# Optimization experiments

Hardware: AMD Instinct MI355X
Metric: run time of the kernel (lower is better)

## Reference

```python
import jax, jax.numpy as jnp
import numpy as np

EPS = 1e-5  # BatchNorm2d eps; BN in eval mode with running_mean=0, running_var=1

def conv_bn_relu(x, W, g, b):
    # x: [B, Cin, N, K]; W: [Cout, Cin] (1x1 conv). BN eval: (y-0)/sqrt(1+eps)*g + b, then ReLU.
    y = jnp.einsum('oc,bcnk->bonk', W, x)
    scale = (g / jnp.sqrt(1.0 + EPS))[None, :, None, None]
    return jax.nn.relu(y * scale + b[None, :, None, None])

def gather_neighbour(pc, idx):
    # pc: [B, N, d]; idx: [B, N, K] -> [B, N, K, d]
    B, N, K = idx.shape
    flat = idx.reshape(B, N * K, 1)
    return jnp.take_along_axis(pc, flat, axis=1).reshape(B, N, K, pc.shape[-1])

def setup_inputs() -> dict:
    B, N, K, D, H = 4, 40960, 16, 64, 32  # H = D // rfa_param
    key = jax.random.key(0)
    ks = jax.random.split(key, 16)
    inp = {
        'feature': jax.random.normal(ks[0], (B, D, N, 1), jnp.float32),
        'xyz': jax.random.normal(ks[1], (B, N, 3), jnp.float32),
        'neigh_idx': jax.random.randint(ks[2], (B, N, K), 0, N, jnp.int64),
        'W1': jax.random.normal(ks[3], (H, 10), jnp.float32) * 0.1,
        'W2': jax.random.normal(ks[4], (H, D), jnp.float32) * 0.1,
        'W3': jax.random.normal(ks[5], (H, 2 * H), jnp.float32) * 0.1,
        'W4': jax.random.normal(ks[6], (D, 2 * H), jnp.float32) * 0.1,
    }
    for i, h in zip(range(1, 5), (H, H, H, D)):
        inp[f'g{i}'] = jax.random.uniform(ks[6 + i], (h,), jnp.float32) + 0.5
        inp[f'b{i}'] = jax.random.normal(ks[10 + i], (h,), jnp.float32) * 0.1
    return inp

def reference(feature, xyz, W1, g1, b1, W2, g2, b2, W3, g3, b3, W4, g4, b4, neigh_idx):
    B, N, K = neigh_idx.shape
    # relative position encoding -> [B, N, K, 10]
    neighbor_xyz = gather_neighbour(xyz, neigh_idx)
    xyz_tile = jnp.broadcast_to(xyz[:, :, None, :], (B, N, K, 3))
    relative_xyz = xyz_tile - neighbor_xyz
    relative_dis = jnp.sqrt(jnp.sum(relative_xyz ** 2, axis=-1, keepdims=True))
    f_xyz = jnp.concatenate([relative_dis, relative_xyz, xyz_tile, neighbor_xyz], axis=-1)
    f_xyz = jnp.transpose(f_xyz, (0, 3, 1, 2))          # [B, 10, N, K]
    f_xyz = conv_bn_relu(f_xyz, W1, g1, b1)             # [B, H, N, K]
    f = conv_bn_relu(feature, W2, g2, b2)               # [B, H, N, 1]
    f_pts = jnp.transpose(f[..., 0], (0, 2, 1))         # [B, N, H]
    f_neighbours = gather_neighbour(f_pts, neigh_idx)   # [B, N, K, H]
    f_neighbours = jnp.transpose(f_neighbours, (0, 3, 1, 2))  # [B, H, N, K]
    f_concat = jnp.concatenate([f_neighbours, f_xyz], axis=1)  # [B, 2H, N, K]
    f_concat = conv_bn_relu(f_concat, W3, g3, b3)       # [B, H, N, K]
    f_concat = jnp.max(f_concat, axis=3, keepdims=True)  # max pooling over neighbors
    f = jnp.concatenate([f_concat, f], axis=1)          # [B, 2H, N, 1]
    return conv_bn_relu(f, W4, g4, b4)                  # [B, D, N, 1]
```

## Files before the change

kernel.cpp:

```cpp
#include <hip/hip_runtime.h>
#include <math.h>

typedef __bf16 bf16_t;
typedef bf16_t bf16x8 __attribute__((ext_vector_type(8)));
typedef bf16_t bf16x4 __attribute__((ext_vector_type(4)));
typedef float  f32x4  __attribute__((ext_vector_type(4)));

#define MFMA16(a, b, c) __builtin_amdgcn_mfma_f32_16x16x32_bf16(a, b, c, 0, 0, 0)

constexpr float BN_INV = 0.999995000037499687f;
constexpr int G2 = 2;

__global__ __launch_bounds__(256) void rfa_k1(
    const float* __restrict__ feature, const float* __restrict__ xyz,
    const float* __restrict__ W2,
    const float* __restrict__ g2, const float* __restrict__ b2,
    bf16_t* __restrict__ fbf, float4* __restrict__ xyz4,
    int N, int nwaves)
{
    int gtid = blockIdx.x * 256 + threadIdx.x;
    int w = gtid >> 6, lane = gtid & 63;
    if (w >= nwaves) return;
    int pt = lane & 15, quad = lane >> 4;
    int T0 = w * 64;
    int b  = T0 / N;
    int n0 = T0 - b * N;

    {
        size_t p = (size_t)T0 + lane;
        xyz4[p] = make_float4(xyz[p * 3], xyz[p * 3 + 1], xyz[p * 3 + 2], 0.f);
    }

    bf16x8 A[2][2];
    #pragma unroll
    for (int mt = 0; mt < 2; ++mt) {
        int h = mt * 16 + pt;
        float sc = g2[h] * BN_INV;
        #pragma unroll
        for (int ks = 0; ks < 2; ++ks) {
            const float* src = W2 + h * 64 + ks * 32 + quad * 8;
            bf16x8 v;
            #pragma unroll
            for (int j = 0; j < 8; ++j) v[j] = (bf16_t)(src[j] * sc);
            A[mt][ks] = v;
        }
    }
    float b2r[8];
    #pragma unroll
    for (int mt = 0; mt < 2; ++mt)
        #pragma unroll
        for (int r = 0; r < 4; ++r) b2r[mt * 4 + r] = b2[mt * 16 + quad * 4 + r];

    const float* fb = feature + (size_t)b * 64 * N;

    #pragma unroll
    for (int g = 0; g < 4; ++g) {
        int nn = n0 + g * 16 + pt;
        size_t T = (size_t)T0 + g * 16 + pt;
        bf16x8 Bf[2];
        #pragma unroll
        for (int ks = 0; ks < 2; ++ks) {
            bf16x8 v;
            #pragma unroll
            for (int j = 0; j < 8; ++j)
                v[j] = (bf16_t)fb[(size_t)(ks * 32 + quad * 8 + j) * N + nn];
            Bf[ks] = v;
        }
        f32x4 acc[2] = {f32x4{0,0,0,0}, f32x4{0,0,0,0}};
        #pragma unroll
        for (int mt = 0; mt < 2; ++mt) {
            acc[mt] = MFMA16(A[mt][0], Bf[0], acc[mt]);
            acc[mt] = MFMA16(A[mt][1], Bf[1], acc[mt]);
        }
        #pragma unroll
        for (int mt = 0; mt < 2; ++mt) {
            bf16x4 o;
            #pragma unroll
            for (int r = 0; r < 4; ++r)
                o[r] = (bf16_t)fmaxf(acc[mt][r] + b2r[mt * 4 + r], 0.f);
            *(bf16x4*)(fbf + T * 32 + mt * 16 + quad * 4) = o;
        }
    }
}

__global__ __launch_bounds__(256) void rfa_k2(
    const float4* __restrict__ xyz4, const int* __restrict__ nidx,
    const float* __restrict__ W1, const float* __restrict__ g1, const float* __restrict__ b1,
    const float* __restrict__ W3, const float* __restrict__ g3, const float* __restrict__ b3,
    const float* __restrict__ W4, const float* __restrict__ g4, const float* __restrict__ b4,
    const bf16_t* __restrict__ fbf, float* __restrict__ out,
    int N, int ngroups)
{
    __shared__ __align__(16) bf16_t sW4[8 * 64 * 8];
    __shared__ float sB[4][32 * 18];

    int tid = threadIdx.x;
    for (int s = tid; s < 512; s += 256) {
        int f = s >> 6, l = s & 63;
        int mt = f >> 1, ks = f & 1, nn = l & 15, q = l >> 4;
        int o = mt * 16 + nn;
        float sc = g4[o] * BN_INV;
        const float* src = W4 + o * 64 + ks * 32 + q * 8;
        bf16x8 v;
        #pragma unroll
        for (int j = 0; j < 8; ++j) v[j] = (bf16_t)(src[j] * sc);
        *(bf16x8*)(sW4 + s * 8) = v;
    }
    __syncthreads();

    int lane = tid & 63, wv = tid >> 6;
    int n = lane & 15, quad = lane >> 4;

    bf16x8 A3[2][2];
    #pragma unroll
    for (int mt = 0; mt < 2; ++mt) {
        int h = mt * 16 + n;
        float sc = g3[h] * BN_INV;
        #pragma unroll
        for (int ks = 0; ks < 2; ++ks) {
            const float* src = W3 + h * 64 + ks * 32 + quad * 8;
            bf16x8 v;
            #pragma unroll
            for (int j = 0; j < 8; ++j) v[j] = (bf16_t)(src[j] * sc);
            A3[mt][ks] = v;
        }
    }
    float a8[8], V0[8], V1[8], V2[8];
    #pragma unroll
    for (int j = 0; j < 8; ++j) {
        int c = quad * 8 + j;
        float s1 = g1[c] * BN_INV;
        const float* wp = W1 + c * 10;
        a8[j] = wp[0] * s1;
        V0[j] = (wp[7] - wp[1]) * s1;
        V1[j] = (wp[8] - wp[2]) * s1;
        V2[j] = (wp[9] - wp[3]) * s1;
    }
    float b3r[8];
    #pragma unroll
    for (int mt = 0; mt < 2; ++mt)
        #pragma unroll
        for (int r = 0; r < 4; ++r) b3r[mt * 4 + r] = b3[mt * 16 + quad * 4 + r];

    float* bounce = sB[wv];
    int wave_id = blockIdx.x * 4 + wv;

    for (int gi = 0; gi < G2; ++gi) {
        int grp = wave_id * G2 + gi;
        if (grp >= ngroups) break;
        int t0 = grp * 16;
        int b = t0 / N;
        int base = b * N;
        int nloc = t0 - base;

        float4 ps = xyz4[(size_t)t0 + n];
        float hoist[8];
        #pragma unroll
        for (int j = 0; j < 8; ++j) {
            int c = quad * 8 + j;
            float s1 = g1[c] * BN_INV;
            const float* wp = W1 + c * 10;
            hoist[j] = b1[c] + ((wp[1] + wp[4]) * ps.x + (wp[2] + wp[5]) * ps.y +
                                (wp[3] + wp[6]) * ps.z) * s1;
        }
        int4 myidx = *(const int4*)(nidx + (size_t)(t0 + n) * 16 + quad * 4);
        bf16x8 Bs = *(const bf16x8*)(fbf + (size_t)(t0 + n) * 32 + quad * 8);

        f32x4 mx0 = {-3.0e38f, -3.0e38f, -3.0e38f, -3.0e38f};
        f32x4 mx1 = {-3.0e38f, -3.0e38f, -3.0e38f, -3.0e38f};

        #pragma unroll
        for (int k = 0; k < 16; ++k) {
            const int comp = k & 3;
            int src = (comp == 0) ? myidx.x : (comp == 1) ? myidx.y
                     : (comp == 2) ? myidx.z : myidx.w;
            int j = __builtin_amdgcn_ds_bpermute(n * 4 + (k >> 2) * 64, src);

            float4 pn = xyz4[(size_t)base + j];
            float rx = ps.x - pn.x, ry = ps.y - pn.y, rz = ps.z - pn.z;
            float dist = sqrtf(rx * rx + ry * ry + rz * rz);

            bf16x8 Bx;
            #pragma unroll
            for (int c = 0; c < 8; ++c) {
                float v = hoist[c] + a8[c] * dist;
                v = fmaf(V0[c], pn.x, v);
                v = fmaf(V1[c], pn.y, v);
                v = fmaf(V2[c], pn.z, v);
                Bx[c] = (bf16_t)fmaxf(v, 0.f);
            }
            bf16x8 Bj = *(const bf16x8*)(fbf + (size_t)(base + j) * 32 + quad * 8);

            f32x4 ac0 = {0,0,0,0}, ac1 = {0,0,0,0};
            ac0 = MFMA16(A3[0][0], Bj, ac0);
            ac0 = MFMA16(A3[0][1], Bx, ac0);
            ac1 = MFMA16(A3[1][0], Bj, ac1);
            ac1 = MFMA16(A3[1][1], Bx, ac1);
            #pragma unroll
            for (int r = 0; r < 4; ++r) {
                mx0[r] = fmaxf(mx0[r], ac0[r]);
                mx1[r] = fmaxf(mx1[r], ac1[r]);
            }
        }

        #pragma unroll
        for (int r = 0; r < 4; ++r) {
            bounce[(quad * 4 + r) * 18 + n]      = fmaxf(mx0[r] + b3r[r], 0.f);
            bounce[(16 + quad * 4 + r) * 18 + n] = fmaxf(mx1[r] + b3r[4 + r], 0.f);
        }
        asm volatile("s_waitcnt lgkmcnt(0)" ::: "memory");
        bf16x8 Bm;
        #pragma unroll
        for (int jj = 0; jj < 8; ++jj)
            Bm[jj] = (bf16_t)bounce[(quad * 8 + jj) * 18 + n];

        #pragma unroll
        for (int mt = 0; mt < 4; ++mt) {
            bf16x8 A40 = *(const bf16x8*)(sW4 + ((size_t)(mt * 2 + 0) * 64 + lane) * 8);
            bf16x8 A41 = *(const bf16x8*)(sW4 + ((size_t)(mt * 2 + 1) * 64 + lane) * 8);
            f32x4 acc = {0,0,0,0};
            acc = MFMA16(A40, Bm, acc);
            acc = MFMA16(A41, Bs, acc);
            #pragma unroll
            for (int r = 0; r < 4; ++r) {
                int o = mt * 16 + quad * 4 + r;
                out[((size_t)b * 64 + o) * N + nloc + n] = fmaxf(acc[r] + b4[o], 0.f);
            }
        }
        asm volatile("s_waitcnt lgkmcnt(0)" ::: "memory");
    }
}

extern "C" void kernel_launch(void* const* d_in, const int* in_sizes, int n_in,
                              void* d_out, int out_size, void* d_ws, size_t ws_size,
                              hipStream_t stream) {
    const float* feature = (const float*)d_in[0];
    const float* xyz     = (const float*)d_in[1];
    const int*   nidx    = (const int*)  d_in[2];
    const float* W1      = (const float*)d_in[3];
    const float* W2      = (const float*)d_in[4];
    const float* W3      = (const float*)d_in[5];
    const float* W4      = (const float*)d_in[6];
    const float* g1 = (const float*)d_in[7];
    const float* b1 = (const float*)d_in[8];
    const float* g2 = (const float*)d_in[9];
    const float* b2 = (const float*)d_in[10];
    const float* g3 = (const float*)d_in[11];
    const float* b3 = (const float*)d_in[12];
    const float* g4 = (const float*)d_in[13];
    const float* b4 = (const float*)d_in[14];
    float* out = (float*)d_out;

    const int B = 4;
    const int N = in_sizes[1] / (B * 3);
    const int total = B * N;

    bf16_t* fbf  = (bf16_t*)d_ws;
    float4* xyz4 = (float4*)((char*)d_ws + (size_t)total * 32 * sizeof(bf16_t));

    const int nw1 = total / 64;
    const int blk1 = (nw1 + 3) / 4;
    const int ngroups = total / 16;
    const int nw2 = (ngroups + G2 - 1) / G2;
    const int blk2 = (nw2 + 3) / 4;

    rfa_k1<<<blk1, 256, 0, stream>>>(feature, xyz, W2, g2, b2, fbf, xyz4, N, nw1);
    rfa_k2<<<blk2, 256, 0, stream>>>(xyz4, nidx, W1, g1, b1, W3, g3, b3, W4, g4, b4,
                                     fbf, out, N, ngroups);
}
```

Before: 193.5 us.

## Interleave features and xyz into 128-byte records and prefetch neighbour gathers

Packs each point's bf16 feature vector (64 B) and padded xyz (16 B) into one 128-byte record, so a neighbour gather touches a single cache line instead of two separate arrays. Each lane now loads all 16 neighbour indices directly instead of exchanging them through ds_bpermute, and the gathers are double-buffered two steps ahead of the MFMA compute to hide memory latency. The cost is more registers for the index array and prefetch buffers, plus padding bytes in the workspace.

```diff
diff --git a/kernel.cpp b/kernel.cpp
--- a/kernel.cpp
+++ b/kernel.cpp
@@ -10,13 +10,13 @@
 
 constexpr float BN_INV = 0.999995000037499687f;
 constexpr int G2 = 2;
+constexpr int RECB = 128;
 
 __global__ __launch_bounds__(256) void rfa_k1(
     const float* __restrict__ feature, const float* __restrict__ xyz,
     const float* __restrict__ W2,
     const float* __restrict__ g2, const float* __restrict__ b2,
-    bf16_t* __restrict__ fbf, float4* __restrict__ xyz4,
-    int N, int nwaves)
+    char* __restrict__ rec, int N, int nwaves)
 {
     int gtid = blockIdx.x * 256 + threadIdx.x;
     int w = gtid >> 6, lane = gtid & 63;
@@ -28,7 +28,8 @@
 
     {
         size_t p = (size_t)T0 + lane;
-        xyz4[p] = make_float4(xyz[p * 3], xyz[p * 3 + 1], xyz[p * 3 + 2], 0.f);
+        float4 v = make_float4(xyz[p * 3], xyz[p * 3 + 1], xyz[p * 3 + 2], 0.f);
+        *(float4*)(rec + p * RECB + 64) = v;
     }
 
     bf16x8 A[2][2];
@@ -78,18 +79,17 @@
             #pragma unroll
             for (int r = 0; r < 4; ++r)
                 o[r] = (bf16_t)fmaxf(acc[mt][r] + b2r[mt * 4 + r], 0.f);
-            *(bf16x4*)(fbf + T * 32 + mt * 16 + quad * 4) = o;
+            *(bf16x4*)(rec + T * RECB + (mt * 16 + quad * 4) * 2) = o;
         }
     }
 }
 
 __global__ __launch_bounds__(256) void rfa_k2(
-    const float4* __restrict__ xyz4, const int* __restrict__ nidx,
+    const char* __restrict__ rec, const int* __restrict__ nidx,
     const float* __restrict__ W1, const float* __restrict__ g1, const float* __restrict__ b1,
     const float* __restrict__ W3, const float* __restrict__ g3, const float* __restrict__ b3,
     const float* __restrict__ W4, const float* __restrict__ g4, const float* __restrict__ b4,
-    const bf16_t* __restrict__ fbf, float* __restrict__ out,
-    int N, int ngroups)
+    float* __restrict__ out, int N, int ngroups)
 {
     __shared__ __align__(16) bf16_t sW4[8 * 64 * 8];
     __shared__ float sB[4][32 * 18];
@@ -136,11 +136,6 @@
         V1[j] = (wp[8] - wp[2]) * s1;
         V2[j] = (wp[9] - wp[3]) * s1;
     }
-    float b3r[8];
-    #pragma unroll
-    for (int mt = 0; mt < 2; ++mt)
-        #pragma unroll
-        for (int r = 0; r < 4; ++r) b3r[mt * 4 + r] = b3[mt * 16 + quad * 4 + r];
 
     float* bounce = sB[wv];
     int wave_id = blockIdx.x * 4 + wv;
@@ -153,7 +148,10 @@
         int base = b * N;
         int nloc = t0 - base;
 
-        float4 ps = xyz4[(size_t)t0 + n];
+        const char* recb  = rec + (size_t)base * RECB;
+        const char* selfr = rec + (size_t)(t0 + n) * RECB;
+
+        float4 ps = *(const float4*)(selfr + 64);
         float hoist[8];
         #pragma unroll
         for (int j = 0; j < 8; ++j) {
@@ -163,33 +161,46 @@
             hoist[j] = b1[c] + ((wp[1] + wp[4]) * ps.x + (wp[2] + wp[5]) * ps.y +
                                 (wp[3] + wp[6]) * ps.z) * s1;
         }
-        int4 myidx = *(const int4*)(nidx + (size_t)(t0 + n) * 16 + quad * 4);
-        bf16x8 Bs = *(const bf16x8*)(fbf + (size_t)(t0 + n) * 32 + quad * 8);
+
+        int j16[16];
+        #pragma unroll
+        for (int q4 = 0; q4 < 4; ++q4) {
+            int4 v = *(const int4*)(nidx + (size_t)(t0 + n) * 16 + q4 * 4);
+            j16[q4 * 4 + 0] = v.x; j16[q4 * 4 + 1] = v.y;
+            j16[q4 * 4 + 2] = v.z; j16[q4 * 4 + 3] = v.w;
+        }
+
+        bf16x8 fj[2]; float4 pn[2];
+        {
+            const char* rp0 = recb + (size_t)j16[0] * RECB;
+            const char* rp1 = recb + (size_t)j16[1] * RECB;
+            fj[0] = *(const bf16x8*)(rp0 + quad * 16);
+            pn[0] = *(const float4*)(rp0 + 64);
+            fj[1] = *(const bf16x8*)(rp1 + quad * 16);
+            pn[1] = *(const float4*)(rp1 + 64);
+        }
 
         f32x4 mx0 = {-3.0e38f, -3.0e38f, -3.0e38f, -3.0e38f};
         f32x4 mx1 = {-3.0e38f, -3.0e38f, -3.0e38f, -3.0e38f};
 
         #pragma unroll
         for (int k = 0; k < 16; ++k) {
-            const int comp = k & 3;
-            int src = (comp == 0) ? myidx.x : (comp == 1) ? myidx.y
-                     : (comp == 2) ? myidx.z : myidx.w;
-            int j = __builtin_amdgcn_ds_bpermute(n * 4 + (k >> 2) * 64, src);
-
-            float4 pn = xyz4[(size_t)base + j];
-            float rx = ps.x - pn.x, ry = ps.y - pn.y, rz = ps.z - pn.z;
+            int s = k & 1;
+            float4 p = pn[s];
+            bf16x8 Bj = fj[s];
+
+            float rx = ps.x - p.x, ry = ps.y - p.y, rz = ps.z - p.z;
             float dist = sqrtf(rx * rx + ry * ry + rz * rz);
 
             bf16x8 Bx;
             #pragma unroll
             for (int c = 0; c < 8; ++c) {
-                float v = hoist[c] + a8[c] * dist;
-                v = fmaf(V0[c], pn.x, v);
-                v = fmaf(V1[c], pn.y, v);
-                v = fmaf(V2[c], pn.z, v);
+                float v = fmaf(a8[c], dist, hoist[c]);
+                v = fmaf(V0[c], p.x, v);
+                v = fmaf(V1[c], p.y, v);
+                v = fmaf(V2[c], p.z, v);
                 Bx[c] = (bf16_t)fmaxf(v, 0.f);
             }
-            bf16x8 Bj = *(const bf16x8*)(fbf + (size_t)(base + j) * 32 + quad * 8);
 
             f32x4 ac0 = {0,0,0,0}, ac1 = {0,0,0,0};
             ac0 = MFMA16(A3[0][0], Bj, ac0);
@@ -201,7 +212,19 @@
                 mx0[r] = fmaxf(mx0[r], ac0[r]);
                 mx1[r] = fmaxf(mx1[r], ac1[r]);
             }
-        }
+
+            if (k + 2 < 16) {
+                const char* rp = recb + (size_t)j16[k + 2] * RECB;
+                fj[s] = *(const bf16x8*)(rp + quad * 16);
+                pn[s] = *(const float4*)(rp + 64);
+            }
+        }
+
+        float b3r[8];
+        #pragma unroll
+        for (int mt = 0; mt < 2; ++mt)
+            #pragma unroll
+            for (int r = 0; r < 4; ++r) b3r[mt * 4 + r] = b3[mt * 16 + quad * 4 + r];
 
         #pragma unroll
         for (int r = 0; r < 4; ++r) {
@@ -213,6 +236,8 @@
         #pragma unroll
         for (int jj = 0; jj < 8; ++jj)
             Bm[jj] = (bf16_t)bounce[(quad * 8 + jj) * 18 + n];
+
+        bf16x8 Bs = *(const bf16x8*)(selfr + quad * 16);
 
         #pragma unroll
         for (int mt = 0; mt < 4; ++mt) {
@@ -255,8 +280,7 @@
     const int N = in_sizes[1] / (B * 3);
     const int total = B * N;
 
-    bf16_t* fbf  = (bf16_t*)d_ws;
-    float4* xyz4 = (float4*)((char*)d_ws + (size_t)total * 32 * sizeof(bf16_t));
+    char* rec = (char*)d_ws;
 
     const int nw1 = total / 64;
     const int blk1 = (nw1 + 3) / 4;
@@ -264,7 +288,7 @@
     const int nw2 = (ngroups + G2 - 1) / G2;
     const int blk2 = (nw2 + 3) / 4;
 
-    rfa_k1<<<blk1, 256, 0, stream>>>(feature, xyz, W2, g2, b2, fbf, xyz4, N, nw1);
-    rfa_k2<<<blk2, 256, 0, stream>>>(xyz4, nidx, W1, g1, b1, W3, g3, b3, W4, g4, b4,
-                                     fbf, out, N, ngroups);
+    rfa_k1<<<blk1, 256, 0, stream>>>(feature, xyz, W2, g2, b2, rec, N, nw1);
+    rfa_k2<<<blk2, 256, 0, stream>>>(rec, nidx, W1, g1, b1, W3, g3, b3, W4, g4, b4,
+                                     out, N, ngroups);
 }
```

Result: slower. 206.6 us (+6.7%).

## Prefetch neighbour gathers four ahead and assign one group per wave with batch-interleaved blocks

Applied to the files above, without the earlier changes.

Each wave now handles a single 16-point group instead of looping over two. The neighbour index row is loaded directly per lane rather than broadcast through ds_bpermute. Feature and xyz gathers are issued four neighbours ahead in a rotating register buffer so memory latency overlaps the MFMA work. Blocks are mapped so consecutive block IDs alternate across batches, and there are twice as many blocks. The aim is to hide gather latency and raise memory-level parallelism, at the cost of more registers and duplicated per-block setup for the weights.

```diff
diff --git a/kernel.cpp b/kernel.cpp
--- a/kernel.cpp
+++ b/kernel.cpp
@@ -9,7 +9,6 @@
 #define MFMA16(a, b, c) __builtin_amdgcn_mfma_f32_16x16x32_bf16(a, b, c, 0, 0, 0)
 
 constexpr float BN_INV = 0.999995000037499687f;
-constexpr int G2 = 2;
 
 __global__ __launch_bounds__(256) void rfa_k1(
     const float* __restrict__ feature, const float* __restrict__ xyz,
@@ -84,12 +83,12 @@
 }
 
 __global__ __launch_bounds__(256) void rfa_k2(
-    const float4* __restrict__ xyz4, const int* __restrict__ nidx,
+    const bf16_t* __restrict__ fbf, const float4* __restrict__ xyz4,
+    const int* __restrict__ nidx,
     const float* __restrict__ W1, const float* __restrict__ g1, const float* __restrict__ b1,
     const float* __restrict__ W3, const float* __restrict__ g3, const float* __restrict__ b3,
     const float* __restrict__ W4, const float* __restrict__ g4, const float* __restrict__ b4,
-    const bf16_t* __restrict__ fbf, float* __restrict__ out,
-    int N, int ngroups)
+    float* __restrict__ out, int N)
 {
     __shared__ __align__(16) bf16_t sW4[8 * 64 * 8];
     __shared__ float sB[4][32 * 18];
@@ -111,6 +110,13 @@
     int lane = tid & 63, wv = tid >> 6;
     int n = lane & 15, quad = lane >> 4;
 
+    int blk  = blockIdx.x;
+    int b    = (blk & 7) >> 1;
+    int slot = (blk >> 3) * 2 + (blk & 1);
+    int grp  = slot * 4 + wv;
+    int nloc = grp * 16;
+    int base = b * N;
+
     bf16x8 A3[2][2];
     #pragma unroll
     for (int mt = 0; mt < 2; ++mt) {
@@ -136,6 +142,76 @@
         V1[j] = (wp[8] - wp[2]) * s1;
         V2[j] = (wp[9] - wp[3]) * s1;
     }
+
+    const bf16_t* fb  = fbf  + (size_t)base * 32;
+    const float4* xzb = xyz4 + (size_t)base;
+    size_t tg = (size_t)base + nloc + n;
+
+    float4 ps = xyz4[tg];
+    float hoist[8];
+    #pragma unroll
+    for (int j = 0; j < 8; ++j) {
+        int c = quad * 8 + j;
+        float s1 = g1[c] * BN_INV;
+        const float* wp = W1 + c * 10;
+        hoist[j] = b1[c] + ((wp[1] + wp[4]) * ps.x + (wp[2] + wp[5]) * ps.y +
+                            (wp[3] + wp[6]) * ps.z) * s1;
+    }
+
+    int j16[16];
+    #pragma unroll
+    for (int q4 = 0; q4 < 4; ++q4) {
+        int4 v = *(const int4*)(nidx + tg * 16 + q4 * 4);
+        j16[q4 * 4 + 0] = v.x; j16[q4 * 4 + 1] = v.y;
+        j16[q4 * 4 + 2] = v.z; j16[q4 * 4 + 3] = v.w;
+    }
+
+    bf16x8 fj[4]; float4 pn[4];
+    #pragma unroll
+    for (int s = 0; s < 4; ++s) {
+        fj[s] = *(const bf16x8*)(fb + (size_t)j16[s] * 32 + quad * 8);
+        pn[s] = xzb[j16[s]];
+    }
+
+    f32x4 mx0 = {-3.0e38f, -3.0e38f, -3.0e38f, -3.0e38f};
+    f32x4 mx1 = {-3.0e38f, -3.0e38f, -3.0e38f, -3.0e38f};
+
+    #pragma unroll
+    for (int k = 0; k < 16; ++k) {
+        int s = k & 3;
+        float4 p = pn[s];
+        bf16x8 Bj = fj[s];
+
+        float rx = ps.x - p.x, ry = ps.y - p.y, rz = ps.z - p.z;
+        float dist = sqrtf(rx * rx + ry * ry + rz * rz);
+
+        bf16x8 Bx;
+        #pragma unroll
+        for (int c = 0; c < 8; ++c) {
+            float v = fmaf(a8[c], dist, hoist[c]);
+            v = fmaf(V0[c], p.x, v);
+            v = fmaf(V1[c], p.y, v);
+            v = fmaf(V2[c], p.z, v);
+            Bx[c] = (bf16_t)fmaxf(v, 0.f);
+        }
+
+        f32x4 ac0 = {0,0,0,0}, ac1 = {0,0,0,0};
+        ac0 = MFMA16(A3[0][0], Bj, ac0);
+        ac0 = MFMA16(A3[0][1], Bx, ac0);
+        ac1 = MFMA16(A3[1][0], Bj, ac1);
+        ac1 = MFMA16(A3[1][1], Bx, ac1);
+        #pragma unroll
+        for (int r = 0; r < 4; ++r) {
+            mx0[r] = fmaxf(mx0[r], ac0[r]);
+            mx1[r] = fmaxf(mx1[r], ac1[r]);
+        }
+
+        if (k + 4 < 16) {
+            fj[s] = *(const bf16x8*)(fb + (size_t)j16[k + 4] * 32 + quad * 8);
+            pn[s] = xzb[j16[k + 4]];
+        }
+    }
+
     float b3r[8];
     #pragma unroll
     for (int mt = 0; mt < 2; ++mt)
@@ -143,91 +219,31 @@
         for (int r = 0; r < 4; ++r) b3r[mt * 4 + r] = b3[mt * 16 + quad * 4 + r];
 
     float* bounce = sB[wv];
-    int wave_id = blockIdx.x * 4 + wv;
-
-    for (int gi = 0; gi < G2; ++gi) {
-        int grp = wave_id * G2 + gi;
-        if (grp >= ngroups) break;
-        int t0 = grp * 16;
-        int b = t0 / N;
-        int base = b * N;
-        int nloc = t0 - base;
-
-        float4 ps = xyz4[(size_t)t0 + n];
-        float hoist[8];
-        #pragma unroll
-        for (int j = 0; j < 8; ++j) {
-            int c = quad * 8 + j;
-            float s1 = g1[c] * BN_INV;
-            const float* wp = W1 + c * 10;
-            hoist[j] = b1[c] + ((wp[1] + wp[4]) * ps.x + (wp[2] + wp[5]) * ps.y +
-                                (wp[3] + wp[6]) * ps.z) * s1;
-        }
-        int4 myidx = *(const int4*)(nidx + (size_t)(t0 + n) * 16 + quad * 4);
-        bf16x8 Bs = *(const bf16x8*)(fbf + (size_t)(t0 + n) * 32 + quad * 8);
-
-        f32x4 mx0 = {-3.0e38f, -3.0e38f, -3.0e38f, -3.0e38f};
-        f32x4 mx1 = {-3.0e38f, -3.0e38f, -3.0e38f, -3.0e38f};
-
-        #pragma unroll
-        for (int k = 0; k < 16; ++k) {
-            const int comp = k & 3;
-            int src = (comp == 0) ? myidx.x : (comp == 1) ? myidx.y
-                     : (comp == 2) ? myidx.z : myidx.w;
-            int j = __builtin_amdgcn_ds_bpermute(n * 4 + (k >> 2) * 64, src);
-
-            float4 pn = xyz4[(size_t)base + j];
-            float rx = ps.x - pn.x, ry = ps.y - pn.y, rz = ps.z - pn.z;
-            float dist = sqrtf(rx * rx + ry * ry + rz * rz);
-
-            bf16x8 Bx;
-            #pragma unroll
-            for (int c = 0; c < 8; ++c) {
-                float v = hoist[c] + a8[c] * dist;
-                v = fmaf(V0[c], pn.x, v);
-                v = fmaf(V1[c], pn.y, v);
-                v = fmaf(V2[c], pn.z, v);
-                Bx[c] = (bf16_t)fmaxf(v, 0.f);
-            }
-            bf16x8 Bj = *(const bf16x8*)(fbf + (size_t)(base + j) * 32 + quad * 8);
-
-            f32x4 ac0 = {0,0,0,0}, ac1 = {0,0,0,0};
-            ac0 = MFMA16(A3[0][0], Bj, ac0);
-            ac0 = MFMA16(A3[0][1], Bx, ac0);
-            ac1 = MFMA16(A3[1][0], Bj, ac1);
-            ac1 = MFMA16(A3[1][1], Bx, ac1);
-            #pragma unroll
-            for (int r = 0; r < 4; ++r) {
-                mx0[r] = fmaxf(mx0[r], ac0[r]);
-                mx1[r] = fmaxf(mx1[r], ac1[r]);
-            }
-        }
-
+    #pragma unroll
+    for (int r = 0; r < 4; ++r) {
+        bounce[(quad * 4 + r) * 18 + n]      = fmaxf(mx0[r] + b3r[r], 0.f);
+        bounce[(16 + quad * 4 + r) * 18 + n] = fmaxf(mx1[r] + b3r[4 + r], 0.f);
+    }
+    asm volatile("s_waitcnt lgkmcnt(0)" ::: "memory");
+    bf16x8 Bm;
+    #pragma unroll
+    for (int jj = 0; jj < 8; ++jj)
+        Bm[jj] = (bf16_t)bounce[(quad * 8 + jj) * 18 + n];
+
+    bf16x8 Bs = *(const bf16x8*)(fb + (size_t)(nloc + n) * 32 + quad * 8);
+
+    #pragma unroll
+    for (int mt = 0; mt < 4; ++mt) {
+        bf16x8 A40 = *(const bf16x8*)(sW4 + ((size_t)(mt * 2 + 0) * 64 + lane) * 8);
+        bf16x8 A41 = *(const bf16x8*)(sW4 + ((size_t)(mt * 2 + 1) * 64 + lane) * 8);
+        f32x4 acc = {0,0,0,0};
+        acc = MFMA16(A40, Bm, acc);
+        acc = MFMA16(A41, Bs, acc);
         #pragma unroll
         for (int r = 0; r < 4; ++r) {
-            bounce[(quad * 4 + r) * 18 + n]      = fmaxf(mx0[r] + b3r[r], 0.f);
-            bounce[(16 + quad * 4 + r) * 18 + n] = fmaxf(mx1[r] + b3r[4 + r], 0.f);
-        }
-        asm volatile("s_waitcnt lgkmcnt(0)" ::: "memory");
-        bf16x8 Bm;
-        #pragma unroll
-        for (int jj = 0; jj < 8; ++jj)
-            Bm[jj] = (bf16_t)bounce[(quad * 8 + jj) * 18 + n];
-
-        #pragma unroll
-        for (int mt = 0; mt < 4; ++mt) {
-            bf16x8 A40 = *(const bf16x8*)(sW4 + ((size_t)(mt * 2 + 0) * 64 + lane) * 8);
-            bf16x8 A41 = *(const bf16x8*)(sW4 + ((size_t)(mt * 2 + 1) * 64 + lane) * 8);
-            f32x4 acc = {0,0,0,0};
-            acc = MFMA16(A40, Bm, acc);
-            acc = MFMA16(A41, Bs, acc);
-            #pragma unroll
-            for (int r = 0; r < 4; ++r) {
-                int o = mt * 16 + quad * 4 + r;
-                out[((size_t)b * 64 + o) * N + nloc + n] = fmaxf(acc[r] + b4[o], 0.f);
-            }
-        }
-        asm volatile("s_waitcnt lgkmcnt(0)" ::: "memory");
+            int o = mt * 16 + quad * 4 + r;
+            out[((size_t)b * 64 + o) * N + nloc + n] = fmaxf(acc[r] + b4[o], 0.f);
+        }
     }
 }
 
@@ -260,11 +276,9 @@
 
     const int nw1 = total / 64;
     const int blk1 = (nw1 + 3) / 4;
-    const int ngroups = total / 16;
-    const int nw2 = (ngroups + G2 - 1) / G2;
-    const int blk2 = (nw2 + 3) / 4;
+    const int blk2 = total / 64;
 
     rfa_k1<<<blk1, 256, 0, stream>>>(feature, xyz, W2, g2, b2, fbf, xyz4, N, nw1);
-    rfa_k2<<<blk2, 256, 0, stream>>>(xyz4, nidx, W1, g1, b1, W3, g3, b3, W4, g4, b4,
-                                     fbf, out, N, ngroups);
+    rfa_k2<<<blk2, 256, 0, stream>>>(fbf, xyz4, nidx, W1, g1, b1, W3, g3, b3,
+                                     W4, g4, b4, out, N);
 }
```

Result: slower. 229.3 us (+18.5%).
